# Performance work log

Hardware: AMD Instinct MI355X
Metric: run time of the kernel (lower is better)

## Reference

```python
import jax, jax.numpy as jnp
import numpy as np

KQ_D = 64  # head dim from init_kwargs

def setup_inputs() -> dict:
    key = jax.random.key(0)
    k1, k2, k3, k4 = jax.random.split(key, 4)
    B, H, S, D = 2, 12, 2048, KQ_D
    q = jax.random.normal(k1, (B, H, S, D), dtype=jnp.float32)
    k = jax.random.normal(k2, (B, H, S, D), dtype=jnp.float32)
    v = jax.random.normal(k3, (B, H, S, D), dtype=jnp.float32)
    mask = jax.random.randint(k4, (B, 1, S, S), 0, 2, dtype=jnp.int32)
    return {"q": q, "k": k, "v": v, "mask": mask}

def reference(q, k, v, mask):
    # attn = (q @ k^T) / sqrt(kq_d)
    scale = 1.0 / (KQ_D ** 0.5)
    attn = jnp.einsum('bhqd,bhkd->bhqk', q, k) * scale
    # masked_fill(mask == 0, -1e9)
    attn = jnp.where(mask == 0, jnp.float32(-1e9), attn)
    # softmax over keys; dropout is identity in eval/reference mode
    attn = jax.nn.softmax(attn, axis=-1)
    out = jnp.einsum('bhqk,bhkd->bhqd', attn, v)
    return out
```

## Files before the change

kernel.cpp:

```cpp
#include <hip/hip_runtime.h>
#include <hip/hip_bf16.h>

#define S_LEN 2048
#define D_DIM 64
#define NH    12
#define NB    2
#define BH_N  (NB*NH)
#define TILES 32
#define TILE_BYTES 16384
#define KV_WS_BYTES ((size_t)BH_N * TILES * TILE_BYTES)
#define MASK_WORDS  ((size_t)NB * S_LEN * TILES)
#define WS_NEEDED   (KV_WS_BYTES + MASK_WORDS * 8)

typedef __attribute__((ext_vector_type(8))) short short8;
typedef __attribute__((ext_vector_type(4))) float f32x4;

static __device__ inline unsigned bfbits(float f) {
    __hip_bfloat16 h = __float2bfloat16(f);
    return (unsigned)*reinterpret_cast<const unsigned short*>(&h);
}

static __device__ inline void gload_lds16(const void* g, unsigned ldsoff) {
    __builtin_amdgcn_global_load_lds(
        (__attribute__((address_space(1))) void*)(unsigned long long)(uintptr_t)g,
        (__attribute__((address_space(3))) void*)(unsigned long long)ldsoff,
        16, 0, 0);
}

__global__ __launch_bounds__(256) void prep(const float* __restrict__ k,
                                            const float* __restrict__ v,
                                            const int* __restrict__ mask,
                                            char* __restrict__ wsKV,
                                            unsigned long long* __restrict__ wm) {
    __shared__ __align__(16) float sv[64 * 68];
    const int tid = threadIdx.x;
    const int bid = blockIdx.x;
    if (bid < 768) {
        const int t = bid & 31, bh = bid >> 5;
        const int kv0 = t * 64;
        const float* kb = k + (size_t)bh * (S_LEN * D_DIM);
        const float* vb = v + (size_t)bh * (S_LEN * D_DIM);
        char* img = wsKV + ((size_t)bh * TILES + t) * TILE_BYTES;

#pragma unroll
        for (int g = 0; g < 4; ++g) {
            int i = g * 256 + tid;
            int row = i >> 4, cb = (i & 15) << 3;
            int cp = cb ^ ((row & 7) << 4);
            float4 f = *(const float4*)(kb + (size_t)(kv0 + row) * D_DIM + (cp >> 1));
            uint2 u;
            u.x = bfbits(f.x) | (bfbits(f.y) << 16);
            u.y = bfbits(f.z) | (bfbits(f.w) << 16);
            *(uint2*)(img + (size_t)i * 8) = u;
            float4 fv = *(const float4*)(vb + (size_t)(kv0 + row) * D_DIM + ((i & 15) << 2));
            *(float4*)&sv[row * 68 + ((i & 15) << 2)] = fv;
        }
        __syncthreads();
#pragma unroll
        for (int g = 0; g < 4; ++g) {
            int i = g * 256 + tid;
            int drow = i >> 4, cb = (i & 15) << 3;
            int cp = cb ^ ((drow & 7) << 4);
            int key0 = cp >> 1;
            uint2 u;
            u.x = bfbits(sv[(key0 + 0) * 68 + drow]) | (bfbits(sv[(key0 + 1) * 68 + drow]) << 16);
            u.y = bfbits(sv[(key0 + 2) * 68 + drow]) | (bfbits(sv[(key0 + 3) * 68 + drow]) << 16);
            *(uint2*)(img + 8192 + (size_t)i * 8) = u;
        }
    } else {
        const int lane = tid & 63;
        const int wgid = (bid - 768) * 4 + (tid >> 6);
#pragma unroll 1
        for (int g = 0; g < 16; ++g) {
            const int t0 = wgid * 64 + g * 4;
            const size_t base = (size_t)t0 * 64 + lane;
            int m0 = mask[base];
            int m1 = mask[base + 64];
            int m2 = mask[base + 128];
            int m3 = mask[base + 192];
            unsigned long long b0 = __ballot(m0 != 0);
            unsigned long long b1 = __ballot(m1 != 0);
            unsigned long long b2 = __ballot(m2 != 0);
            unsigned long long b3 = __ballot(m3 != 0);
            if (lane == 0) {
                wm[t0 + 0] = b0; wm[t0 + 1] = b1;
                wm[t0 + 2] = b2; wm[t0 + 3] = b3;
            }
        }
    }
}

__global__ __launch_bounds__(256, 3) void attn_main(
    const float* __restrict__ q, const char* __restrict__ wsKV,
    const unsigned long long* __restrict__ wm, float* __restrict__ out)
{
    __shared__ __align__(16) char smem[2 * TILE_BYTES + 8192];

    const int tid  = threadIdx.x;
    const int wave = tid >> 6;
    const int lane = tid & 63;
    const int l16  = lane & 15;
    const int lhi  = lane >> 4;

    const int f  = blockIdx.x;
    const int n  = (f & 7) * 96 + (f >> 3);
    const int bx = n & 31;
    const int bh = n >> 5;
    const int b  = bh / NH;
    const int qw = bx * 64 + wave * 16;
    const int qq = qw + l16;

    const float* qb = q + (size_t)bh * (S_LEN * D_DIM);
    float*       ob = out + (size_t)bh * (S_LEN * D_DIM);
    const char*  tileBase = wsKV + (size_t)bh * TILES * TILE_BYTES;
    const size_t widx = ((size_t)b * S_LEN + qq) * TILES;

    const float PRE = 0.125f * 1.44269504088896f;

    short8 bq[2];
#pragma unroll
    for (int ks = 0; ks < 2; ++ks) {
        const float* src = qb + (size_t)qq * D_DIM + ks * 32 + lhi * 8;
        float4 f0 = *(const float4*)(src);
        float4 f1 = *(const float4*)(src + 4);
        short8 a;
        a[0] = (short)bfbits(f0.x * PRE); a[1] = (short)bfbits(f0.y * PRE);
        a[2] = (short)bfbits(f0.z * PRE); a[3] = (short)bfbits(f0.w * PRE);
        a[4] = (short)bfbits(f1.x * PRE); a[5] = (short)bfbits(f1.y * PRE);
        a[6] = (short)bfbits(f1.z * PRE); a[7] = (short)bfbits(f1.w * PRE);
        bq[ks] = a;
    }

    f32x4 o[4];
#pragma unroll
    for (int dt = 0; dt < 4; ++dt) o[dt] = (f32x4){0.f, 0.f, 0.f, 0.f};
    float lsum = 0.f;

    const unsigned smem_base = (unsigned)(uintptr_t)(&smem[0]);
    char* pw = smem + 2 * TILE_BYTES + wave * 2048;

    f32x4 scA[4], scB[4];
    short8 vA[2][4], vB[2][4];
    unsigned long long mwA, mwB;

#define QKL(SC, VV, RB) { \
    const char* sK_  = smem + (RB) * TILE_BYTES; \
    const char* sVt_ = sK_ + 8192; \
    _Pragma("unroll") \
    for (int tt = 0; tt < 4; ++tt) SC[tt] = (f32x4){0.f, 0.f, 0.f, 0.f}; \
    _Pragma("unroll") \
    for (int ks = 0; ks < 2; ++ks) { \
        _Pragma("unroll") \
        for (int tt = 0; tt < 4; ++tt) { \
            int row = tt * 16 + l16; \
            int byte = row * 128 + ((ks * 64 + lhi * 16) ^ ((row & 7) << 4)); \
            short8 ak = *(const short8*)(sK_ + byte); \
            SC[tt] = __builtin_amdgcn_mfma_f32_16x16x32_bf16(ak, bq[ks], SC[tt], 0, 0, 0); \
        } \
    } \
    _Pragma("unroll") \
    for (int ks = 0; ks < 2; ++ks) \
        _Pragma("unroll") \
        for (int dt = 0; dt < 4; ++dt) { \
            int drow = dt * 16 + l16; \
            int vbyte = drow * 128 + ((ks * 64 + lhi * 16) ^ ((drow & 7) << 4)); \
            VV[ks][dt] = *(const short8*)(sVt_ + vbyte); \
        } }

#define FIN(SC, VV, MW) { \
    float rs = 0.f; \
    _Pragma("unroll") \
    for (int tt = 0; tt < 4; ++tt) { \
        unsigned nib = (unsigned)((MW) >> (tt * 16 + lhi * 4)) & 0xFu; \
        _Pragma("unroll") \
        for (int r = 0; r < 4; ++r) { \
            float p = ((nib >> r) & 1u) ? exp2f(SC[tt][r]) : 0.f; \
            SC[tt][r] = p; \
            rs += p; \
        } \
    } \
    lsum += rs; \
    _Pragma("unroll") \
    for (int tt = 0; tt < 4; ++tt) { \
        uint2 u; \
        u.x = bfbits(SC[tt][0]) | (bfbits(SC[tt][1]) << 16); \
        u.y = bfbits(SC[tt][2]) | (bfbits(SC[tt][3]) << 16); \
        int byte = l16 * 128 + (((tt * 16 + lhi * 4) * 2) ^ ((l16 & 7) << 4)); \
        *(uint2*)(pw + byte) = u; \
    } \
    _Pragma("unroll") \
    for (int ks = 0; ks < 2; ++ks) { \
        int pbyte = l16 * 128 + ((ks * 64 + lhi * 16) ^ ((l16 & 7) << 4)); \
        short8 pa = *(const short8*)(pw + pbyte); \
        _Pragma("unroll") \
        for (int dt = 0; dt < 4; ++dt) \
            o[dt] = __builtin_amdgcn_mfma_f32_16x16x32_bf16(pa, VV[ks][dt], o[dt], 0, 0, 0); \
    } }

#define ITER(I_, RB, SCN, VVN, MWN, SCP, VVP, MWP) { \
    if ((I_) < 31) { \
        const char* timg = tileBase + (size_t)((I_) + 1) * TILE_BYTES; \
        unsigned dstb = smem_base + (unsigned)((((I_) + 1) & 1) * TILE_BYTES); \
        _Pragma("unroll") \
        for (int j = 0; j < 4; ++j) { \
            unsigned off = (unsigned)(wave * 4096 + j * 1024 + lane * 16); \
            gload_lds16(timg + off, dstb + off); \
        } \
    } \
    MWN = wm[widx + (I_)]; \
    QKL(SCN, VVN, RB) \
    FIN(SCP, VVP, MWP) \
    __syncthreads(); }

#pragma unroll
    for (int j = 0; j < 4; ++j) {
        unsigned off = (unsigned)(wave * 4096 + j * 1024 + lane * 16);
        gload_lds16(tileBase + off, smem_base + off);
    }
    __syncthreads();
    {
        const char* timg = tileBase + (size_t)1 * TILE_BYTES;
        unsigned dstb = smem_base + (unsigned)TILE_BYTES;
#pragma unroll
        for (int j = 0; j < 4; ++j) {
            unsigned off = (unsigned)(wave * 4096 + j * 1024 + lane * 16);
            gload_lds16(timg + off, dstb + off);
        }
    }
    mwA = wm[widx];
    QKL(scA, vA, 0)
    __syncthreads();

    int i = 1;
#pragma unroll 1
    for (int th = 0; th < 15; ++th) {
        ITER(i,     1, scB, vB, mwB, scA, vA, mwA)
        ITER(i + 1, 0, scA, vA, mwA, scB, vB, mwB)
        i += 2;
    }
    ITER(31, 1, scB, vB, mwB, scA, vA, mwA)
    FIN(scB, vB, mwB)

#undef ITER
#undef FIN
#undef QKL

    lsum += __shfl_xor(lsum, 16);
    lsum += __shfl_xor(lsum, 32);
    float invl = 1.0f / lsum;
    float ir[4];
#pragma unroll
    for (int r = 0; r < 4; ++r) ir[r] = __shfl(invl, lhi * 4 + r);
#pragma unroll
    for (int dt = 0; dt < 4; ++dt)
#pragma unroll
        for (int r = 0; r < 4; ++r) {
            int qrow = qw + lhi * 4 + r;
            int dcol = dt * 16 + l16;
            ob[(size_t)qrow * D_DIM + dcol] = o[dt][r] * ir[r];
        }
}

__global__ __launch_bounds__(256, 3) void attn_fallback(
    const float* __restrict__ q, const float* __restrict__ k,
    const float* __restrict__ v, const int* __restrict__ mask,
    float* __restrict__ out)
{
    __shared__ __align__(16) unsigned short sK[4096];
    __shared__ __align__(16) unsigned short sVt[4096];
    __shared__ __align__(16) unsigned short sP[4096];

    const int tid  = threadIdx.x;
    const int wave = tid >> 6;
    const int lane = tid & 63;
    const int l16  = lane & 15;
    const int lhi  = lane >> 4;

    const int bh = blockIdx.y;
    const int b  = bh / NH;
    const int q0 = blockIdx.x * 64;
    const int qw = q0 + wave * 16;
    const int qq = qw + l16;

    const float* qbase = q + (size_t)bh * S_LEN * D_DIM;
    const float* kbase = k + (size_t)bh * S_LEN * D_DIM;
    const float* vbase = v + (size_t)bh * S_LEN * D_DIM;
    const int*   mp = mask + (size_t)b * S_LEN * S_LEN + (size_t)qq * S_LEN;

    const float PRE = 0.125f * 1.44269504088896f;

    short8 bq[2];
#pragma unroll
    for (int ks = 0; ks < 2; ++ks) {
        const float* src = qbase + (size_t)qq * D_DIM + ks * 32 + lhi * 8;
        float4 f0 = *(const float4*)(src);
        float4 f1 = *(const float4*)(src + 4);
        short8 a;
        a[0] = (short)bfbits(f0.x * PRE); a[1] = (short)bfbits(f0.y * PRE);
        a[2] = (short)bfbits(f0.z * PRE); a[3] = (short)bfbits(f0.w * PRE);
        a[4] = (short)bfbits(f1.x * PRE); a[5] = (short)bfbits(f1.y * PRE);
        a[6] = (short)bfbits(f1.z * PRE); a[7] = (short)bfbits(f1.w * PRE);
        bq[ks] = a;
    }

    f32x4 o[4];
#pragma unroll
    for (int dt = 0; dt < 4; ++dt) o[dt] = (f32x4){0.f, 0.f, 0.f, 0.f};
    float mrun = -1e30f, lrun = 0.f;
    unsigned short* pw = sP + wave * 1024;

    int srow[4], sd[4];
#pragma unroll
    for (int s = 0; s < 4; ++s) { int i = tid + 256 * s; srow[s] = i >> 4; sd[s] = (i & 15) * 4; }

    float4 kreg[4], vreg[4];
#pragma unroll
    for (int s = 0; s < 4; ++s) {
        kreg[s] = *(const float4*)(kbase + (size_t)srow[s] * D_DIM + sd[s]);
        vreg[s] = *(const float4*)(vbase + (size_t)srow[s] * D_DIM + sd[s]);
    }

    for (int kv0 = 0; kv0 < S_LEN; kv0 += 64) {
        __syncthreads();
#pragma unroll
        for (int s = 0; s < 4; ++s) {
            unsigned p0 = bfbits(kreg[s].x) | (bfbits(kreg[s].y) << 16);
            unsigned p1 = bfbits(kreg[s].z) | (bfbits(kreg[s].w) << 16);
            int byte = srow[s] * 128 + ((sd[s] * 2) ^ ((srow[s] & 7) << 4));
            *(uint2*)((char*)sK + byte) = make_uint2(p0, p1);
        }
#pragma unroll
        for (int s = 0; s < 4; ++s) {
            float ff[4] = {vreg[s].x, vreg[s].y, vreg[s].z, vreg[s].w};
#pragma unroll
            for (int jj = 0; jj < 4; ++jj) {
                int dd = sd[s] + jj;
                int byte = dd * 128 + ((srow[s] * 2) ^ ((dd & 7) << 4));
                *(unsigned short*)((char*)sVt + byte) = (unsigned short)bfbits(ff[jj]);
            }
        }
        __syncthreads();

        if (kv0 + 64 < S_LEN) {
#pragma unroll
            for (int s = 0; s < 4; ++s) {
                kreg[s] = *(const float4*)(kbase + (size_t)(kv0 + 64 + srow[s]) * D_DIM + sd[s]);
                vreg[s] = *(const float4*)(vbase + (size_t)(kv0 + 64 + srow[s]) * D_DIM + sd[s]);
            }
        }

        int4 m0 = *(const int4*)(mp + kv0 + lhi * 4);
        int4 m1 = *(const int4*)(mp + kv0 + 16 + lhi * 4);
        int4 m2 = *(const int4*)(mp + kv0 + 32 + lhi * 4);
        int4 m3 = *(const int4*)(mp + kv0 + 48 + lhi * 4);

        f32x4 sc[4];
#pragma unroll
        for (int tt = 0; tt < 4; ++tt) sc[tt] = (f32x4){0.f, 0.f, 0.f, 0.f};
#pragma unroll
        for (int ks = 0; ks < 2; ++ks) {
#pragma unroll
            for (int tt = 0; tt < 4; ++tt) {
                int row = tt * 16 + l16;
                int byte = row * 128 + ((ks * 64 + lhi * 16) ^ ((row & 7) << 4));
                short8 ak = *(const short8*)((const char*)sK + byte);
                sc[tt] = __builtin_amdgcn_mfma_f32_16x16x32_bf16(ak, bq[ks], sc[tt], 0, 0, 0);
            }
        }

        const int4 mm[4] = {m0, m1, m2, m3};
        float pm = -1e30f;
#pragma unroll
        for (int tt = 0; tt < 4; ++tt)
#pragma unroll
            for (int r = 0; r < 4; ++r) {
                float s = ((const int*)&mm[tt])[r] ? sc[tt][r] : -1e9f;
                sc[tt][r] = s;
                pm = fmaxf(pm, s);
            }
        pm = fmaxf(pm, __shfl_xor(pm, 16));
        pm = fmaxf(pm, __shfl_xor(pm, 32));

        float mnew = fmaxf(mrun, pm);
        float fsc = exp2f(mrun - mnew);
        mrun = mnew;
        float rs = 0.f;
#pragma unroll
        for (int tt = 0; tt < 4; ++tt)
#pragma unroll
            for (int r = 0; r < 4; ++r) {
                float p = exp2f(sc[tt][r] - mnew);
                sc[tt][r] = p;
                rs += p;
            }
        rs += __shfl_xor(rs, 16);
        rs += __shfl_xor(rs, 32);
        lrun = lrun * fsc + rs;

        float fr[4];
#pragma unroll
        for (int r = 0; r < 4; ++r) fr[r] = __shfl(fsc, lhi * 4 + r);
#pragma unroll
        for (int dt = 0; dt < 4; ++dt)
#pragma unroll
            for (int r = 0; r < 4; ++r) o[dt][r] *= fr[r];

#pragma unroll
        for (int tt = 0; tt < 4; ++tt) {
            unsigned p0 = bfbits(sc[tt][0]) | (bfbits(sc[tt][1]) << 16);
            unsigned p1 = bfbits(sc[tt][2]) | (bfbits(sc[tt][3]) << 16);
            int byte = l16 * 128 + (((tt * 16 + lhi * 4) * 2) ^ ((l16 & 7) << 4));
            *(uint2*)((char*)pw + byte) = make_uint2(p0, p1);
        }

#pragma unroll
        for (int ks = 0; ks < 2; ++ks) {
            int pbyte = l16 * 128 + ((ks * 64 + lhi * 16) ^ ((l16 & 7) << 4));
            short8 pa = *(const short8*)((const char*)pw + pbyte);
#pragma unroll
            for (int dt = 0; dt < 4; ++dt) {
                int drow = dt * 16 + l16;
                int vbyte = drow * 128 + ((ks * 64 + lhi * 16) ^ ((drow & 7) << 4));
                short8 bv = *(const short8*)((const char*)sVt + vbyte);
                o[dt] = __builtin_amdgcn_mfma_f32_16x16x32_bf16(pa, bv, o[dt], 0, 0, 0);
            }
        }
    }

    float invl = 1.0f / lrun;
    float ir[4];
#pragma unroll
    for (int r = 0; r < 4; ++r) ir[r] = __shfl(invl, lhi * 4 + r);
#pragma unroll
    for (int dt = 0; dt < 4; ++dt)
#pragma unroll
        for (int r = 0; r < 4; ++r) {
            int qrow = qw + lhi * 4 + r;
            int dcol = dt * 16 + l16;
            out[(size_t)bh * S_LEN * D_DIM + (size_t)qrow * D_DIM + dcol] = o[dt][r] * ir[r];
        }
}

extern "C" void kernel_launch(void* const* d_in, const int* in_sizes, int n_in,
                              void* d_out, int out_size, void* d_ws, size_t ws_size,
                              hipStream_t stream) {
    const float* q   = (const float*)d_in[0];
    const float* k   = (const float*)d_in[1];
    const float* v   = (const float*)d_in[2];
    const int* mask  = (const int*)d_in[3];
    float* out = (float*)d_out;

    if (ws_size >= WS_NEEDED) {
        char* ws = (char*)d_ws;
        char* wsKV = ws;
        unsigned long long* wm = (unsigned long long*)(ws + KV_WS_BYTES);
        prep<<<dim3(1280), dim3(256), 0, stream>>>(k, v, mask, wsKV, wm);
        attn_main<<<dim3(768), dim3(256), 0, stream>>>(q, wsKV, wm, out);
    } else {
        attn_fallback<<<dim3(S_LEN / 64, BH_N), dim3(256), 0, stream>>>(q, k, v, mask, out);
    }
}
```

Measured before the change: 74.19 us.

## Double-buffer two-tile KV chunks and drop software-pipelined QK/PV interleave

The attention main loop now loads 32KB chunks (two KV tiles) per stage into double-buffered LDS and processes both tiles per barrier. This halves the number of barriers but removes the register-level interleave of the next tile's QK with the previous tile's PV. Occupancy drops from 3 to 2 blocks per CU because of the doubled LDS. Bf16 conversion now uses a paired pack intrinsic, and masked scores go through exp2 of -1e9 instead of a select to zero.

```diff
diff --git a/kernel.cpp b/kernel.cpp
--- a/kernel.cpp
+++ b/kernel.cpp
@@ -8,6 +8,7 @@
 #define BH_N  (NB*NH)
 #define TILES 32
 #define TILE_BYTES 16384
+#define CHUNK_BYTES 32768
 #define KV_WS_BYTES ((size_t)BH_N * TILES * TILE_BYTES)
 #define MASK_WORDS  ((size_t)NB * S_LEN * TILES)
 #define WS_NEEDED   (KV_WS_BYTES + MASK_WORDS * 8)
@@ -18,6 +19,11 @@
 static __device__ inline unsigned bfbits(float f) {
     __hip_bfloat16 h = __float2bfloat16(f);
     return (unsigned)*reinterpret_cast<const unsigned short*>(&h);
+}
+
+static __device__ inline unsigned bfpack2(float a, float b) {
+    __hip_bfloat162 h = __float22bfloat162_rn(make_float2(a, b));
+    return *reinterpret_cast<const unsigned*>(&h);
 }
 
 static __device__ inline void gload_lds16(const void* g, unsigned ldsoff) {
@@ -49,8 +55,8 @@
             int cp = cb ^ ((row & 7) << 4);
             float4 f = *(const float4*)(kb + (size_t)(kv0 + row) * D_DIM + (cp >> 1));
             uint2 u;
-            u.x = bfbits(f.x) | (bfbits(f.y) << 16);
-            u.y = bfbits(f.z) | (bfbits(f.w) << 16);
+            u.x = bfpack2(f.x, f.y);
+            u.y = bfpack2(f.z, f.w);
             *(uint2*)(img + (size_t)i * 8) = u;
             float4 fv = *(const float4*)(vb + (size_t)(kv0 + row) * D_DIM + ((i & 15) << 2));
             *(float4*)&sv[row * 68 + ((i & 15) << 2)] = fv;
@@ -63,8 +69,8 @@
             int cp = cb ^ ((drow & 7) << 4);
             int key0 = cp >> 1;
             uint2 u;
-            u.x = bfbits(sv[(key0 + 0) * 68 + drow]) | (bfbits(sv[(key0 + 1) * 68 + drow]) << 16);
-            u.y = bfbits(sv[(key0 + 2) * 68 + drow]) | (bfbits(sv[(key0 + 3) * 68 + drow]) << 16);
+            u.x = bfpack2(sv[(key0 + 0) * 68 + drow], sv[(key0 + 1) * 68 + drow]);
+            u.y = bfpack2(sv[(key0 + 2) * 68 + drow], sv[(key0 + 3) * 68 + drow]);
             *(uint2*)(img + 8192 + (size_t)i * 8) = u;
         }
     } else {
@@ -90,11 +96,11 @@
     }
 }
 
-__global__ __launch_bounds__(256, 3) void attn_main(
+__global__ __launch_bounds__(256, 2) void attn_main(
     const float* __restrict__ q, const char* __restrict__ wsKV,
     const unsigned long long* __restrict__ wm, float* __restrict__ out)
 {
-    __shared__ __align__(16) char smem[2 * TILE_BYTES + 8192];
+    __shared__ __align__(16) char smem[2 * CHUNK_BYTES + 8192];
 
     const int tid  = threadIdx.x;
     const int wave = tid >> 6;
@@ -137,113 +143,96 @@
     float lsum = 0.f;
 
     const unsigned smem_base = (unsigned)(uintptr_t)(&smem[0]);
-    char* pw = smem + 2 * TILE_BYTES + wave * 2048;
-
-    f32x4 scA[4], scB[4];
-    short8 vA[2][4], vB[2][4];
-    unsigned long long mwA, mwB;
-
-#define QKL(SC, VV, RB) { \
-    const char* sK_  = smem + (RB) * TILE_BYTES; \
-    const char* sVt_ = sK_ + 8192; \
-    _Pragma("unroll") \
-    for (int tt = 0; tt < 4; ++tt) SC[tt] = (f32x4){0.f, 0.f, 0.f, 0.f}; \
-    _Pragma("unroll") \
-    for (int ks = 0; ks < 2; ++ks) { \
+    char* pw = smem + 2 * CHUNK_BYTES + wave * 2048;
+
+#define TILE_WORK(SKB, MW) { \
+        const char* sK_  = (SKB); \
+        const char* sVt_ = sK_ + 8192; \
+        f32x4 sc[4]; \
+        _Pragma("unroll") \
+        for (int tt = 0; tt < 4; ++tt) sc[tt] = (f32x4){0.f, 0.f, 0.f, 0.f}; \
+        _Pragma("unroll") \
+        for (int ks = 0; ks < 2; ++ks) { \
+            _Pragma("unroll") \
+            for (int tt = 0; tt < 4; ++tt) { \
+                int row = tt * 16 + l16; \
+                int byte = row * 128 + ((ks * 64 + lhi * 16) ^ ((row & 7) << 4)); \
+                short8 ak = *(const short8*)(sK_ + byte); \
+                sc[tt] = __builtin_amdgcn_mfma_f32_16x16x32_bf16(ak, bq[ks], sc[tt], 0, 0, 0); \
+            } \
+        } \
+        short8 bvv[2][4]; \
+        _Pragma("unroll") \
+        for (int ks = 0; ks < 2; ++ks) \
+            _Pragma("unroll") \
+            for (int dt = 0; dt < 4; ++dt) { \
+                int drow = dt * 16 + l16; \
+                int vbyte = drow * 128 + ((ks * 64 + lhi * 16) ^ ((drow & 7) << 4)); \
+                bvv[ks][dt] = *(const short8*)(sVt_ + vbyte); \
+            } \
+        float rs = 0.f; \
         _Pragma("unroll") \
         for (int tt = 0; tt < 4; ++tt) { \
-            int row = tt * 16 + l16; \
-            int byte = row * 128 + ((ks * 64 + lhi * 16) ^ ((row & 7) << 4)); \
-            short8 ak = *(const short8*)(sK_ + byte); \
-            SC[tt] = __builtin_amdgcn_mfma_f32_16x16x32_bf16(ak, bq[ks], SC[tt], 0, 0, 0); \
+            unsigned nib = (unsigned)((MW) >> (tt * 16 + lhi * 4)) & 0xFu; \
+            _Pragma("unroll") \
+            for (int r = 0; r < 4; ++r) { \
+                float s = ((nib >> r) & 1u) ? sc[tt][r] : -1e9f; \
+                float p = exp2f(s); \
+                sc[tt][r] = p; \
+                rs += p; \
+            } \
         } \
-    } \
-    _Pragma("unroll") \
-    for (int ks = 0; ks < 2; ++ks) \
-        _Pragma("unroll") \
-        for (int dt = 0; dt < 4; ++dt) { \
-            int drow = dt * 16 + l16; \
-            int vbyte = drow * 128 + ((ks * 64 + lhi * 16) ^ ((drow & 7) << 4)); \
-            VV[ks][dt] = *(const short8*)(sVt_ + vbyte); \
+        lsum += rs; \
+        _Pragma("unroll") \
+        for (int tt = 0; tt < 4; ++tt) { \
+            uint2 u; \
+            u.x = bfpack2(sc[tt][0], sc[tt][1]); \
+            u.y = bfpack2(sc[tt][2], sc[tt][3]); \
+            int byte = l16 * 128 + (((tt * 16 + lhi * 4) * 2) ^ ((l16 & 7) << 4)); \
+            *(uint2*)(pw + byte) = u; \
+        } \
+        _Pragma("unroll") \
+        for (int ks = 0; ks < 2; ++ks) { \
+            int pbyte = l16 * 128 + ((ks * 64 + lhi * 16) ^ ((l16 & 7) << 4)); \
+            short8 pa = *(const short8*)(pw + pbyte); \
+            _Pragma("unroll") \
+            for (int dt = 0; dt < 4; ++dt) \
+                o[dt] = __builtin_amdgcn_mfma_f32_16x16x32_bf16(pa, bvv[ks][dt], o[dt], 0, 0, 0); \
         } }
 
-#define FIN(SC, VV, MW) { \
-    float rs = 0.f; \
-    _Pragma("unroll") \
-    for (int tt = 0; tt < 4; ++tt) { \
-        unsigned nib = (unsigned)((MW) >> (tt * 16 + lhi * 4)) & 0xFu; \
-        _Pragma("unroll") \
-        for (int r = 0; r < 4; ++r) { \
-            float p = ((nib >> r) & 1u) ? exp2f(SC[tt][r]) : 0.f; \
-            SC[tt][r] = p; \
-            rs += p; \
-        } \
-    } \
-    lsum += rs; \
-    _Pragma("unroll") \
-    for (int tt = 0; tt < 4; ++tt) { \
-        uint2 u; \
-        u.x = bfbits(SC[tt][0]) | (bfbits(SC[tt][1]) << 16); \
-        u.y = bfbits(SC[tt][2]) | (bfbits(SC[tt][3]) << 16); \
-        int byte = l16 * 128 + (((tt * 16 + lhi * 4) * 2) ^ ((l16 & 7) << 4)); \
-        *(uint2*)(pw + byte) = u; \
-    } \
-    _Pragma("unroll") \
-    for (int ks = 0; ks < 2; ++ks) { \
-        int pbyte = l16 * 128 + ((ks * 64 + lhi * 16) ^ ((l16 & 7) << 4)); \
-        short8 pa = *(const short8*)(pw + pbyte); \
-        _Pragma("unroll") \
-        for (int dt = 0; dt < 4; ++dt) \
-            o[dt] = __builtin_amdgcn_mfma_f32_16x16x32_bf16(pa, VV[ks][dt], o[dt], 0, 0, 0); \
-    } }
-
-#define ITER(I_, RB, SCN, VVN, MWN, SCP, VVP, MWP) { \
-    if ((I_) < 31) { \
-        const char* timg = tileBase + (size_t)((I_) + 1) * TILE_BYTES; \
-        unsigned dstb = smem_base + (unsigned)((((I_) + 1) & 1) * TILE_BYTES); \
-        _Pragma("unroll") \
-        for (int j = 0; j < 4; ++j) { \
-            unsigned off = (unsigned)(wave * 4096 + j * 1024 + lane * 16); \
-            gload_lds16(timg + off, dstb + off); \
-        } \
-    } \
-    MWN = wm[widx + (I_)]; \
-    QKL(SCN, VVN, RB) \
-    FIN(SCP, VVP, MWP) \
-    __syncthreads(); }
-
-#pragma unroll
-    for (int j = 0; j < 4; ++j) {
-        unsigned off = (unsigned)(wave * 4096 + j * 1024 + lane * 16);
+    unsigned long long mwA = wm[widx];
+    unsigned long long mwB = wm[widx + 1];
+#pragma unroll
+    for (int j = 0; j < 8; ++j) {
+        unsigned off = (unsigned)(j * 4096 + wave * 1024 + lane * 16);
         gload_lds16(tileBase + off, smem_base + off);
     }
     __syncthreads();
-    {
-        const char* timg = tileBase + (size_t)1 * TILE_BYTES;
-        unsigned dstb = smem_base + (unsigned)TILE_BYTES;
-#pragma unroll
-        for (int j = 0; j < 4; ++j) {
-            unsigned off = (unsigned)(wave * 4096 + j * 1024 + lane * 16);
-            gload_lds16(timg + off, dstb + off);
-        }
-    }
-    mwA = wm[widx];
-    QKL(scA, vA, 0)
-    __syncthreads();
-
-    int i = 1;
-#pragma unroll 1
-    for (int th = 0; th < 15; ++th) {
-        ITER(i,     1, scB, vB, mwB, scA, vA, mwA)
-        ITER(i + 1, 0, scA, vA, mwA, scB, vB, mwB)
-        i += 2;
-    }
-    ITER(31, 1, scB, vB, mwB, scA, vA, mwA)
-    FIN(scB, vB, mwB)
-
-#undef ITER
-#undef FIN
-#undef QKL
+
+    int buf = 0;
+    for (int c = 0; c < 16; ++c) {
+        if (c < 15) {
+            const char* csrc = tileBase + (size_t)(c + 1) * CHUNK_BYTES;
+            unsigned dstb = smem_base + (unsigned)((buf ^ 1) * CHUNK_BYTES);
+#pragma unroll
+            for (int j = 0; j < 8; ++j) {
+                unsigned off = (unsigned)(j * 4096 + wave * 1024 + lane * 16);
+                gload_lds16(csrc + off, dstb + off);
+            }
+        }
+        unsigned long long mwA_n = (c < 15) ? wm[widx + 2 * c + 2] : 0ull;
+        unsigned long long mwB_n = (c < 15) ? wm[widx + 2 * c + 3] : 0ull;
+
+        const char* cb = smem + buf * CHUNK_BYTES;
+        TILE_WORK(cb, mwA)
+        TILE_WORK(cb + TILE_BYTES, mwB)
+
+        __syncthreads();
+        buf ^= 1;
+        mwA = mwA_n;
+        mwB = mwB_n;
+    }
+#undef TILE_WORK
 
     lsum += __shfl_xor(lsum, 16);
     lsum += __shfl_xor(lsum, 32);
```

Result: slower. 78.21 us (+5.4%).
